# Kernel optimization log

Measured on AMD Instinct MI355X. Metric: run time of the kernel, lower is better.

The kernel has to match this reference:

```python
import jax, jax.numpy as jnp
import numpy as np

B, S, D, E, K = 4, 4096, 2048, 64, 8
STD = 0.02 / np.sqrt(D)
BIAS_UPDATE_SPEED = 0.001


def setup_inputs() -> dict:
    key = jax.random.key(0)
    k1, k2, k3, k4 = jax.random.split(key, 4)
    return {
        "x": jax.random.normal(k1, (B, S, D), dtype=jnp.float32),
        "Wr": (jax.random.normal(k2, (E, D), dtype=jnp.float32) * STD),
        "Wn": (jax.random.normal(k3, (E, D), dtype=jnp.float32) * STD),
        "bias": jnp.zeros((E,), dtype=jnp.float32),
        "noise_u": jax.random.uniform(k4, (B, S, E), dtype=jnp.float32),
    }


def reference(x, Wr, Wn, bias, noise_u):
    # x: [B,S,D]; Wr, Wn: [E,D]; bias: [E]; noise_u: [B,S,E] uniform(0,1)
    logits = jnp.einsum("bsd,ed->bse", x, Wr)          # router logits
    noisy_logits = jnp.einsum("bsd,ed->bse", x, Wn)    # noise scale logits
    noise = noise_u * jax.nn.softplus(noisy_logits)
    z = noise + logits + bias                           # [B,S,E]

    topk_vals, topk_idx = jax.lax.top_k(z, K)           # [B,S,K]
    neg_inf = jnp.full_like(z, -jnp.inf)
    sparse = jnp.put_along_axis(neg_inf, topk_idx, topk_vals, axis=-1,
                                inplace=False)          # -inf except top-k slots
    probs = jax.nn.softmax(sparse, axis=-1)             # [B,S,E]

    # load-balancing bias update (faithful to source, incl. scalar sum quirk)
    sel_mask = jax.nn.one_hot(topk_idx, E, dtype=jnp.float32).sum(axis=(0, 1, 2))  # [E]
    current_expert_load = sel_mask.sum()                # scalar (as in torch .sum(0) on 1-D)
    total_tokens = B * S * K
    avg_load = total_tokens / E
    load_violation = avg_load - current_expert_load
    new_bias = bias + BIAS_UPDATE_SPEED * jnp.sign(load_violation)

    return probs, topk_idx, new_bias
```

## Files before the change

### kernel.cpp

```cpp
#include <hip/hip_runtime.h>
#include <math.h>

#define BB 4
#define SS 4096
#define DD 2048
#define EE 64
#define KK 8
#define TT_TOTAL (BB*SS)
#define E2 128
#define DK 32
#define NC (DD/DK)

typedef double double2_t __attribute__((ext_vector_type(2)));
typedef double double4_t __attribute__((ext_vector_type(4)));

__device__ __forceinline__ double softplus64(double x) {
    return fmax(x, 0.0) + log1p(exp(-fabs(x)));
}

__device__ __forceinline__ int SW(int c) {
    return c ^ (((c >> 4) & 7) << 1);
}

#define ROW 130

template<int KS>
__launch_bounds__(256, 2)
__global__ void gemm8_kernel(const float* __restrict__ x,
                             const float* __restrict__ Wr,
                             const float* __restrict__ Wn,
                             double* __restrict__ zp)
{
    __shared__ __align__(16) double xs[DK][ROW];
    __shared__ __align__(16) double ws[DK][ROW];

    const int tid   = threadIdx.x;
    const int split = blockIdx.x % KS;
    const int bt    = blockIdx.x / KS;
    const int tok0  = bt * 128;
    const int kbase = split * (DD / KS);
    const int NCH   = (DD / KS) / DK;

    const int stok = tid & 127;
    const int skh  = tid >> 7;
    const int scol = SW(stok);
    const float* xsrc = x + (size_t)(tok0 + stok) * DD + kbase + 16 * skh;
    const float* wsrc = ((stok < EE) ? Wr + (size_t)stok * DD
                                     : Wn + (size_t)(stok - EE) * DD)
                        + kbase + 16 * skh;

    const int og2 = tid & 15;
    const int tg2 = tid >> 4;
    int colx[4], colw[4];
    #pragma unroll
    for (int h = 0; h < 4; ++h) colx[h] = SW(2 * tg2 + 32 * h);
    #pragma unroll
    for (int g = 0; g < 4; ++g) colw[g] = SW(2 * og2 + 32 * g);

    double acc[8][8];
    #pragma unroll
    for (int i = 0; i < 8; ++i)
        #pragma unroll
        for (int j = 0; j < 8; ++j) acc[i][j] = 0.0;

    float4 xr[4], wr[4];
    #pragma unroll
    for (int i = 0; i < 4; ++i) {
        xr[i] = *reinterpret_cast<const float4*>(xsrc + 4 * i);
        wr[i] = *reinterpret_cast<const float4*>(wsrc + 4 * i);
    }

    for (int c = 0; c < NCH; ++c) {
        __syncthreads();

        #pragma unroll
        for (int i = 0; i < 4; ++i) {
            const int k = 16 * skh + 4 * i;
            xs[k+0][scol] = (double)xr[i].x;
            xs[k+1][scol] = (double)xr[i].y;
            xs[k+2][scol] = (double)xr[i].z;
            xs[k+3][scol] = (double)xr[i].w;
            ws[k+0][scol] = (double)wr[i].x;
            ws[k+1][scol] = (double)wr[i].y;
            ws[k+2][scol] = (double)wr[i].z;
            ws[k+3][scol] = (double)wr[i].w;
        }
        __syncthreads();

        if (c + 1 < NCH) {
            const int off = (c + 1) * DK;
            #pragma unroll
            for (int i = 0; i < 4; ++i) {
                xr[i] = *reinterpret_cast<const float4*>(xsrc + off + 4 * i);
                wr[i] = *reinterpret_cast<const float4*>(wsrc + off + 4 * i);
            }
        }

        #pragma unroll 4
        for (int k = 0; k < DK; ++k) {
            double2_t xv[4], wv[4];
            #pragma unroll
            for (int h = 0; h < 4; ++h)
                xv[h] = *reinterpret_cast<const double2_t*>(&xs[k][colx[h]]);
            #pragma unroll
            for (int g = 0; g < 4; ++g)
                wv[g] = *reinterpret_cast<const double2_t*>(&ws[k][colw[g]]);
            #pragma unroll
            for (int h = 0; h < 4; ++h)
                #pragma unroll
                for (int e = 0; e < 2; ++e)
                    #pragma unroll
                    for (int g = 0; g < 4; ++g) {
                        acc[2*h+e][2*g+0] = fma(xv[h][e], wv[g][0], acc[2*h+e][2*g+0]);
                        acc[2*h+e][2*g+1] = fma(xv[h][e], wv[g][1], acc[2*h+e][2*g+1]);
                    }
        }
    }

    double* zbase = zp + (size_t)split * TT_TOTAL * E2;
    #pragma unroll
    for (int h = 0; h < 4; ++h)
        #pragma unroll
        for (int e = 0; e < 2; ++e) {
            const int tok = 2 * tg2 + e + 32 * h;
            double* row = zbase + (size_t)(tok0 + tok) * E2;
            #pragma unroll
            for (int g = 0; g < 4; ++g) {
                double2_t v = {acc[2*h+e][2*g+0], acc[2*h+e][2*g+1]};
                *reinterpret_cast<double2_t*>(&row[2 * og2 + 32 * g]) = v;
            }
        }
}

template<int KS>
__launch_bounds__(256, 4)
__global__ void topk2_kernel(const double* __restrict__ zp,
                             const float* __restrict__ bias,
                             const float* __restrict__ noise_u,
                             float* __restrict__ out_probs,
                             float* __restrict__ out_idx)
{
    const int tid  = threadIdx.x;
    const int wid  = tid >> 6;
    const int lane = tid & 63;
    const int tok0 = blockIdx.x * 32;

    for (int tt = 0; tt < 8; ++tt) {
        const int tok = tok0 + wid * 8 + tt;
        const size_t gtok = (size_t)tok;

        double logit = 0.0, noisy = 0.0;
        #pragma unroll
        for (int s = 0; s < KS; ++s) {
            const double* row = zp + (size_t)s * TT_TOTAL * E2 + (size_t)tok * E2;
            logit += row[lane];
            noisy += row[EE + lane];
        }
        const double zv = (double)noise_u[gtok * EE + lane] * softplus64(noisy)
                          + logit + (double)bias[lane];

        double zw = zv;
        bool   sel = false;
        double m0  = 0.0;
        #pragma unroll
        for (int it = 0; it < KK; ++it) {
            double v  = zw;
            int    ix = lane;
            #pragma unroll
            for (int off = 32; off > 0; off >>= 1) {
                const double ov = __shfl_xor(v, off, 64);
                const int    oi = __shfl_xor(ix, off, 64);
                if (ov > v || (ov == v && oi < ix)) { v = ov; ix = oi; }
            }
            if (it == 0) m0 = v;
            if (lane == ix) { sel = true; zw = -INFINITY; }
            if (lane == 0) out_idx[gtok * KK + it] = (float)ix;
        }

        const double ex = sel ? exp(zv - m0) : 0.0;
        double den = ex;
        #pragma unroll
        for (int off = 32; off > 0; off >>= 1) den += __shfl_xor(den, off, 64);

        out_probs[gtok * EE + lane] = (float)(ex / den);
    }
}

#define BT 32
#define XT 34
#define WT 66

__launch_bounds__(256, 4)
__global__ void gemm_kernel(const float* __restrict__ x,
                            const float* __restrict__ Wr,
                            const float* __restrict__ Wn,
                            double* __restrict__ zout)
{
    __shared__ __align__(16) double xs[DK][XT];
    __shared__ __align__(16) double ws[DK][WT];

    const int tid  = threadIdx.x;
    const int bt   = blockIdx.x >> 1;
    const int be   = blockIdx.x & 1;
    const int tok0 = bt * BT;
    const int e0   = be * 64;

    const int kk = tid & 31;
    const int tq = tid >> 5;
    const float* xsrc[4];
    const float* wsrc[8];
    #pragma unroll
    for (int j = 0; j < 4; ++j)
        xsrc[j] = x + (size_t)(tok0 + 4 * tq + j) * DD + kk;
    #pragma unroll
    for (int j = 0; j < 4; ++j) {
        const int e  = e0 + 4 * tq + j;
        const int e2 = e0 + 32 + 4 * tq + j;
        wsrc[j]     = ((e  < EE) ? Wr + (size_t)e * DD
                                 : Wn + (size_t)(e  - EE) * DD) + kk;
        wsrc[4 + j] = ((e2 < EE) ? Wr + (size_t)e2 * DD
                                 : Wn + (size_t)(e2 - EE) * DD) + kk;
    }

    const int og = tid & 15;
    const int tp = tid >> 4;

    double acc[2][4];
    #pragma unroll
    for (int t = 0; t < 2; ++t)
        #pragma unroll
        for (int i = 0; i < 4; ++i) acc[t][i] = 0.0;

    float xr[4], wr[8];
    #pragma unroll
    for (int j = 0; j < 4; ++j) xr[j] = xsrc[j][0];
    #pragma unroll
    for (int j = 0; j < 8; ++j) wr[j] = wsrc[j][0];

    for (int c = 0; c < NC; ++c) {
        __syncthreads();
        {
            double4_t xv = {(double)xr[0], (double)xr[1], (double)xr[2], (double)xr[3]};
            *reinterpret_cast<double4_t*>(&xs[kk][4 * tq]) = xv;
            double4_t w0 = {(double)wr[0], (double)wr[1], (double)wr[2], (double)wr[3]};
            *reinterpret_cast<double4_t*>(&ws[kk][4 * tq]) = w0;
            double4_t w1 = {(double)wr[4], (double)wr[5], (double)wr[6], (double)wr[7]};
            *reinterpret_cast<double4_t*>(&ws[kk][32 + 4 * tq]) = w1;
        }
        __syncthreads();
        if (c + 1 < NC) {
            const int off = (c + 1) * DK;
            #pragma unroll
            for (int j = 0; j < 4; ++j) xr[j] = xsrc[j][off];
            #pragma unroll
            for (int j = 0; j < 8; ++j) wr[j] = wsrc[j][off];
        }
        #pragma unroll 4
        for (int k = 0; k < DK; ++k) {
            const double2_t xv = *reinterpret_cast<const double2_t*>(&xs[k][2 * tp]);
            const double2_t w0 = *reinterpret_cast<const double2_t*>(&ws[k][2 * og]);
            const double2_t w1 = *reinterpret_cast<const double2_t*>(&ws[k][32 + 2 * og]);
            acc[0][0] = fma(xv.x, w0.x, acc[0][0]);
            acc[0][1] = fma(xv.x, w0.y, acc[0][1]);
            acc[0][2] = fma(xv.x, w1.x, acc[0][2]);
            acc[0][3] = fma(xv.x, w1.y, acc[0][3]);
            acc[1][0] = fma(xv.y, w0.x, acc[1][0]);
            acc[1][1] = fma(xv.y, w0.y, acc[1][1]);
            acc[1][2] = fma(xv.y, w1.x, acc[1][2]);
            acc[1][3] = fma(xv.y, w1.y, acc[1][3]);
        }
    }

    #pragma unroll
    for (int t = 0; t < 2; ++t) {
        const size_t base = (size_t)(tok0 + 2 * tp + t) * E2 + e0;
        double2_t lo = {acc[t][0], acc[t][1]};
        double2_t hi = {acc[t][2], acc[t][3]};
        *reinterpret_cast<double2_t*>(&zout[base + 2 * og])      = lo;
        *reinterpret_cast<double2_t*>(&zout[base + 32 + 2 * og]) = hi;
    }
}

#define F_XT 34
#define F_WR 130
#define F_ZR 130
#define F_SMEM ((DK*F_XT + DK*F_WR)*8)

__launch_bounds__(256, 3)
__global__ void router_kernel(const float* __restrict__ x,
                              const float* __restrict__ Wr,
                              const float* __restrict__ Wn,
                              const float* __restrict__ bias,
                              const float* __restrict__ noise_u,
                              float* __restrict__ out_probs,
                              float* __restrict__ out_idx)
{
    __shared__ __align__(16) char smem_raw[F_SMEM];
    double (*xs)[F_XT] = reinterpret_cast<double(*)[F_XT]>(smem_raw);
    double (*wt)[F_WR] = reinterpret_cast<double(*)[F_WR]>(smem_raw + DK*F_XT*8);
    double (*zbuf)[F_ZR] = reinterpret_cast<double(*)[F_ZR]>(smem_raw);

    const int tid  = threadIdx.x;
    const int tok0 = blockIdx.x * 32;
    const int stok = tid >> 3;
    const int sfi  = tid & 7;
    const float* xsrc = x + (size_t)(tok0 + stok) * DD + sfi * 4;
    const float* wsrc[4];
    #pragma unroll
    for (int it = 0; it < 4; ++it) {
        const int r = it * 32 + stok;
        wsrc[it] = ((r < EE) ? (Wr + (size_t)r * DD)
                             : (Wn + (size_t)(r - EE) * DD)) + sfi * 4;
    }
    const int tg = tid >> 5;
    const int eg = tid & 31;

    double acc[4][4];
    #pragma unroll
    for (int t = 0; t < 4; ++t)
        #pragma unroll
        for (int i = 0; i < 4; ++i) acc[t][i] = 0.0;

    float4 xr  = *reinterpret_cast<const float4*>(xsrc);
    float4 wr0 = *reinterpret_cast<const float4*>(wsrc[0]);
    float4 wr1 = *reinterpret_cast<const float4*>(wsrc[1]);
    float4 wr2 = *reinterpret_cast<const float4*>(wsrc[2]);
    float4 wr3 = *reinterpret_cast<const float4*>(wsrc[3]);

    for (int c = 0; c < NC; ++c) {
        __syncthreads();
        {
            const int k0 = sfi * 4;
            xs[k0+0][stok] = (double)xr.x;  xs[k0+1][stok] = (double)xr.y;
            xs[k0+2][stok] = (double)xr.z;  xs[k0+3][stok] = (double)xr.w;
            wt[k0+0][stok      ] = (double)wr0.x; wt[k0+1][stok      ] = (double)wr0.y;
            wt[k0+2][stok      ] = (double)wr0.z; wt[k0+3][stok      ] = (double)wr0.w;
            wt[k0+0][stok + 32 ] = (double)wr1.x; wt[k0+1][stok + 32 ] = (double)wr1.y;
            wt[k0+2][stok + 32 ] = (double)wr1.z; wt[k0+3][stok + 32 ] = (double)wr1.w;
            wt[k0+0][stok + 64 ] = (double)wr2.x; wt[k0+1][stok + 64 ] = (double)wr2.y;
            wt[k0+2][stok + 64 ] = (double)wr2.z; wt[k0+3][stok + 64 ] = (double)wr2.w;
            wt[k0+0][stok + 96 ] = (double)wr3.x; wt[k0+1][stok + 96 ] = (double)wr3.y;
            wt[k0+2][stok + 96 ] = (double)wr3.z; wt[k0+3][stok + 96 ] = (double)wr3.w;
        }
        __syncthreads();
        if (c + 1 < NC) {
            const int off = (c + 1) * DK;
            xr  = *reinterpret_cast<const float4*>(xsrc + off);
            wr0 = *reinterpret_cast<const float4*>(wsrc[0] + off);
            wr1 = *reinterpret_cast<const float4*>(wsrc[1] + off);
            wr2 = *reinterpret_cast<const float4*>(wsrc[2] + off);
            wr3 = *reinterpret_cast<const float4*>(wsrc[3] + off);
        }
        #pragma unroll 4
        for (int k = 0; k < DK; ++k) {
            const double2_t xv0 = *reinterpret_cast<const double2_t*>(&xs[k][tg * 4]);
            const double2_t xv1 = *reinterpret_cast<const double2_t*>(&xs[k][tg * 4 + 2]);
            const double2_t w0  = *reinterpret_cast<const double2_t*>(&wt[k][2 * eg]);
            const double2_t w1  = *reinterpret_cast<const double2_t*>(&wt[k][64 + 2 * eg]);
            const double xvv[4] = {xv0.x, xv0.y, xv1.x, xv1.y};
            #pragma unroll
            for (int t = 0; t < 4; ++t) {
                acc[t][0] = fma(xvv[t], w0.x, acc[t][0]);
                acc[t][1] = fma(xvv[t], w0.y, acc[t][1]);
                acc[t][2] = fma(xvv[t], w1.x, acc[t][2]);
                acc[t][3] = fma(xvv[t], w1.y, acc[t][3]);
            }
        }
    }
    __syncthreads();
    #pragma unroll
    for (int t = 0; t < 4; ++t) {
        double2_t lo = {acc[t][0], acc[t][1]};
        double2_t hi = {acc[t][2], acc[t][3]};
        *reinterpret_cast<double2_t*>(&zbuf[tg * 4 + t][2 * eg])      = lo;
        *reinterpret_cast<double2_t*>(&zbuf[tg * 4 + t][64 + 2 * eg]) = hi;
    }
    __syncthreads();

    const int wid  = tid >> 6;
    const int lane = tid & 63;
    for (int tt = 0; tt < 8; ++tt) {
        const int tok = wid * 8 + tt;
        const size_t gtok = (size_t)tok0 + tok;
        const double logit = zbuf[tok][lane];
        const double noisy = zbuf[tok][EE + lane];
        const double zv = (double)noise_u[gtok * EE + lane] * softplus64(noisy)
                          + logit + (double)bias[lane];
        double zw = zv;
        bool   sel = false;
        double m0  = 0.0;
        #pragma unroll
        for (int it = 0; it < KK; ++it) {
            double v  = zw;
            int    ix = lane;
            #pragma unroll
            for (int off = 32; off > 0; off >>= 1) {
                const double ov = __shfl_xor(v, off, 64);
                const int    oi = __shfl_xor(ix, off, 64);
                if (ov > v || (ov == v && oi < ix)) { v = ov; ix = oi; }
            }
            if (it == 0) m0 = v;
            if (lane == ix) { sel = true; zw = -INFINITY; }
            if (lane == 0) out_idx[gtok * KK + it] = (float)ix;
        }
        const double ex = sel ? exp(zv - m0) : 0.0;
        double den = ex;
        #pragma unroll
        for (int off = 32; off > 0; off >>= 1) den += __shfl_xor(den, off, 64);
        out_probs[gtok * EE + lane] = (float)(ex / den);
    }
}

__global__ void bias_kernel(const float* __restrict__ bias,
                            float* __restrict__ out_bias)
{
    const int e = threadIdx.x;
    if (e < EE) {
        const double load_violation = (double)(TT_TOTAL * KK) / EE
                                      - (double)(TT_TOTAL * KK);
        const double s = (load_violation > 0.0) ? 1.0
                         : ((load_violation < 0.0) ? -1.0 : 0.0);
        out_bias[e] = bias[e] + (float)(0.001 * s);
    }
}

extern "C" void kernel_launch(void* const* d_in, const int* in_sizes, int n_in,
                              void* d_out, int out_size, void* d_ws, size_t ws_size,
                              hipStream_t stream)
{
    const float* x       = (const float*)d_in[0];
    const float* Wr      = (const float*)d_in[1];
    const float* Wn      = (const float*)d_in[2];
    const float* bias    = (const float*)d_in[3];
    const float* noise_u = (const float*)d_in[4];

    float* out       = (float*)d_out;
    float* out_probs = out;
    float* out_idx   = out + (size_t)TT_TOTAL * EE;
    float* out_bias  = out + (size_t)TT_TOTAL * EE + (size_t)TT_TOTAL * KK;

    const size_t z1 = (size_t)TT_TOTAL * E2 * sizeof(double);

    if (ws_size >= 4 * z1) {
        double* zp = (double*)d_ws;
        gemm8_kernel<4><<<128 * 4, 256, 0, stream>>>(x, Wr, Wn, zp);
        topk2_kernel<4><<<TT_TOTAL / 32, 256, 0, stream>>>(zp, bias, noise_u,
                                                           out_probs, out_idx);
    } else if (ws_size >= 2 * z1) {
        double* zp = (double*)d_ws;
        gemm8_kernel<2><<<128 * 2, 256, 0, stream>>>(x, Wr, Wn, zp);
        topk2_kernel<2><<<TT_TOTAL / 32, 256, 0, stream>>>(zp, bias, noise_u,
                                                           out_probs, out_idx);
    } else if (ws_size >= z1) {
        double* z = (double*)d_ws;
        gemm_kernel<<<(TT_TOTAL / BT) * 2, 256, 0, stream>>>(x, Wr, Wn, z);
        topk2_kernel<1><<<TT_TOTAL / 32, 256, 0, stream>>>(z, bias, noise_u,
                                                           out_probs, out_idx);
    } else {
        router_kernel<<<TT_TOTAL / 32, 256, 0, stream>>>(
            x, Wr, Wn, bias, noise_u, out_probs, out_idx);
    }
    bias_kernel<<<1, 64, 0, stream>>>(bias, out_bias);
}
```

Before: 231.3 us.

## Shrink GEMM token tile to 64, stage fp32 in LDS, raise occupancy

The fp64 router GEMM now works on 64-token tiles instead of 128, which doubles the grid. It stores x and W in shared memory as fp32 and converts them to double in the inner loop. The per-thread accumulator tile drops from 8x8 to 4x8 doubles and launch bounds move from 2 to 4 blocks per CU. The aim is to cut LDS footprint and register pressure so more waves can hide latency. The cost is extra float-to-double conversions in the hot loop, fewer FMAs per LDS read, and more global W traffic per output.

```diff
diff --git a/kernel.cpp b/kernel.cpp
--- a/kernel.cpp
+++ b/kernel.cpp
@@ -22,104 +22,118 @@
     return c ^ (((c >> 4) & 7) << 1);
 }
 
-#define ROW 130
+#define XROWF 66
+#define WROWF 130
 
 template<int KS>
-__launch_bounds__(256, 2)
-__global__ void gemm8_kernel(const float* __restrict__ x,
-                             const float* __restrict__ Wr,
-                             const float* __restrict__ Wn,
-                             double* __restrict__ zp)
-{
-    __shared__ __align__(16) double xs[DK][ROW];
-    __shared__ __align__(16) double ws[DK][ROW];
+__launch_bounds__(256, 4)
+__global__ void gemm64_kernel(const float* __restrict__ x,
+                              const float* __restrict__ Wr,
+                              const float* __restrict__ Wn,
+                              double* __restrict__ zp)
+{
+    __shared__ __align__(16) float xs[DK][XROWF];
+    __shared__ __align__(16) float ws[DK][WROWF];
 
     const int tid   = threadIdx.x;
     const int split = blockIdx.x % KS;
     const int bt    = blockIdx.x / KS;
-    const int tok0  = bt * 128;
+    const int tok0  = bt * 64;
     const int kbase = split * (DD / KS);
     const int NCH   = (DD / KS) / DK;
 
-    const int stok = tid & 127;
-    const int skh  = tid >> 7;
-    const int scol = SW(stok);
-    const float* xsrc = x + (size_t)(tok0 + stok) * DD + kbase + 16 * skh;
-    const float* wsrc = ((stok < EE) ? Wr + (size_t)stok * DD
-                                     : Wn + (size_t)(stok - EE) * DD)
-                        + kbase + 16 * skh;
+    const int xrow = tid & 63;
+    const int xkq  = tid >> 6;
+    const int xc   = SW(xrow);
+    const float* xsrc = x + (size_t)(tok0 + xrow) * DD + kbase + 8 * xkq;
+
+    const int wrow = tid & 127;
+    const int wkh  = tid >> 7;
+    const int wc   = SW(wrow);
+    const float* wsrc = ((wrow < EE) ? Wr + (size_t)wrow * DD
+                                     : Wn + (size_t)(wrow - EE) * DD)
+                        + kbase + 16 * wkh;
 
     const int og2 = tid & 15;
     const int tg2 = tid >> 4;
-    int colx[4], colw[4];
-    #pragma unroll
-    for (int h = 0; h < 4; ++h) colx[h] = SW(2 * tg2 + 32 * h);
-    #pragma unroll
-    for (int g = 0; g < 4; ++g) colw[g] = SW(2 * og2 + 32 * g);
-
-    double acc[8][8];
-    #pragma unroll
-    for (int i = 0; i < 8; ++i)
-        #pragma unroll
-        for (int j = 0; j < 8; ++j) acc[i][j] = 0.0;
-
-    float4 xr[4], wr[4];
-    #pragma unroll
-    for (int i = 0; i < 4; ++i) {
-        xr[i] = *reinterpret_cast<const float4*>(xsrc + 4 * i);
-        wr[i] = *reinterpret_cast<const float4*>(wsrc + 4 * i);
-    }
+    const int cx0 = SW(2 * tg2);
+    const int cx1 = SW(2 * tg2 + 32);
+    int cw[4];
+    #pragma unroll
+    for (int g = 0; g < 4; ++g) cw[g] = SW(2 * og2 + 32 * g);
+
+    double acc[4][8];
+    #pragma unroll
+    for (int t = 0; t < 4; ++t)
+        #pragma unroll
+        for (int o = 0; o < 8; ++o) acc[t][o] = 0.0;
+
+    float4 xa[2], wa[4];
+    #pragma unroll
+    for (int i = 0; i < 2; ++i)
+        xa[i] = *reinterpret_cast<const float4*>(xsrc + 4 * i);
+    #pragma unroll
+    for (int i = 0; i < 4; ++i)
+        wa[i] = *reinterpret_cast<const float4*>(wsrc + 4 * i);
 
     for (int c = 0; c < NCH; ++c) {
         __syncthreads();
 
-        #pragma unroll
-        for (int i = 0; i < 4; ++i) {
-            const int k = 16 * skh + 4 * i;
-            xs[k+0][scol] = (double)xr[i].x;
-            xs[k+1][scol] = (double)xr[i].y;
-            xs[k+2][scol] = (double)xr[i].z;
-            xs[k+3][scol] = (double)xr[i].w;
-            ws[k+0][scol] = (double)wr[i].x;
-            ws[k+1][scol] = (double)wr[i].y;
-            ws[k+2][scol] = (double)wr[i].z;
-            ws[k+3][scol] = (double)wr[i].w;
+        {
+            const int kx = 8 * xkq;
+            xs[kx+0][xc] = xa[0].x;  xs[kx+1][xc] = xa[0].y;
+            xs[kx+2][xc] = xa[0].z;  xs[kx+3][xc] = xa[0].w;
+            xs[kx+4][xc] = xa[1].x;  xs[kx+5][xc] = xa[1].y;
+            xs[kx+6][xc] = xa[1].z;  xs[kx+7][xc] = xa[1].w;
+            const int kw = 16 * wkh;
+            #pragma unroll
+            for (int i = 0; i < 4; ++i) {
+                ws[kw + 4*i + 0][wc] = wa[i].x;
+                ws[kw + 4*i + 1][wc] = wa[i].y;
+                ws[kw + 4*i + 2][wc] = wa[i].z;
+                ws[kw + 4*i + 3][wc] = wa[i].w;
+            }
         }
         __syncthreads();
 
         if (c + 1 < NCH) {
             const int off = (c + 1) * DK;
             #pragma unroll
-            for (int i = 0; i < 4; ++i) {
-                xr[i] = *reinterpret_cast<const float4*>(xsrc + off + 4 * i);
-                wr[i] = *reinterpret_cast<const float4*>(wsrc + off + 4 * i);
-            }
+            for (int i = 0; i < 2; ++i)
+                xa[i] = *reinterpret_cast<const float4*>(xsrc + off + 4 * i);
+            #pragma unroll
+            for (int i = 0; i < 4; ++i)
+                wa[i] = *reinterpret_cast<const float4*>(wsrc + off + 4 * i);
         }
 
         #pragma unroll 4
         for (int k = 0; k < DK; ++k) {
-            double2_t xv[4], wv[4];
-            #pragma unroll
-            for (int h = 0; h < 4; ++h)
-                xv[h] = *reinterpret_cast<const double2_t*>(&xs[k][colx[h]]);
+            const float2 xf0 = *reinterpret_cast<const float2*>(&xs[k][cx0]);
+            const float2 xf1 = *reinterpret_cast<const float2*>(&xs[k][cx1]);
+            float2 wf[4];
             #pragma unroll
             for (int g = 0; g < 4; ++g)
-                wv[g] = *reinterpret_cast<const double2_t*>(&ws[k][colw[g]]);
-            #pragma unroll
-            for (int h = 0; h < 4; ++h)
+                wf[g] = *reinterpret_cast<const float2*>(&ws[k][cw[g]]);
+
+            const double xv[4] = {(double)xf0.x, (double)xf0.y,
+                                  (double)xf1.x, (double)xf1.y};
+            double wv[8];
+            #pragma unroll
+            for (int g = 0; g < 4; ++g) {
+                wv[2*g+0] = (double)wf[g].x;
+                wv[2*g+1] = (double)wf[g].y;
+            }
+            #pragma unroll
+            for (int t = 0; t < 4; ++t)
                 #pragma unroll
-                for (int e = 0; e < 2; ++e)
-                    #pragma unroll
-                    for (int g = 0; g < 4; ++g) {
-                        acc[2*h+e][2*g+0] = fma(xv[h][e], wv[g][0], acc[2*h+e][2*g+0]);
-                        acc[2*h+e][2*g+1] = fma(xv[h][e], wv[g][1], acc[2*h+e][2*g+1]);
-                    }
+                for (int o = 0; o < 8; ++o)
+                    acc[t][o] = fma(xv[t], wv[o], acc[t][o]);
         }
     }
 
     double* zbase = zp + (size_t)split * TT_TOTAL * E2;
     #pragma unroll
-    for (int h = 0; h < 4; ++h)
+    for (int h = 0; h < 2; ++h)
         #pragma unroll
         for (int e = 0; e < 2; ++e) {
             const int tok = 2 * tg2 + e + 32 * h;
@@ -443,12 +457,12 @@
 
     if (ws_size >= 4 * z1) {
         double* zp = (double*)d_ws;
-        gemm8_kernel<4><<<128 * 4, 256, 0, stream>>>(x, Wr, Wn, zp);
+        gemm64_kernel<4><<<256 * 4, 256, 0, stream>>>(x, Wr, Wn, zp);
         topk2_kernel<4><<<TT_TOTAL / 32, 256, 0, stream>>>(zp, bias, noise_u,
                                                            out_probs, out_idx);
     } else if (ws_size >= 2 * z1) {
         double* zp = (double*)d_ws;
-        gemm8_kernel<2><<<128 * 2, 256, 0, stream>>>(x, Wr, Wn, zp);
+        gemm64_kernel<2><<<256 * 2, 256, 0, stream>>>(x, Wr, Wn, zp);
         topk2_kernel<2><<<TT_TOTAL / 32, 256, 0, stream>>>(zp, bias, noise_u,
                                                            out_probs, out_idx);
     } else if (ws_size >= z1) {
```

New measurement: 278.1 us. +20.3%, slower.

## Double-buffer shared-memory tiles in fp64 router GEMM with two-stage prefetch

Applied to the files above, without the earlier changes.

The GEMM kernel now keeps two half-size (16-deep) shared-memory tiles. While it computes on one buffer it writes the next chunk into the other and issues global loads two chunks ahead. This removes one of the two barriers per chunk and lets LDS stores overlap with FMA work. In exchange the chunk loop runs twice as many iterations, each with less work per barrier, and register pressure may rise.

```diff
diff --git a/kernel.cpp b/kernel.cpp
--- a/kernel.cpp
+++ b/kernel.cpp
@@ -22,32 +22,33 @@
     return c ^ (((c >> 4) & 7) << 1);
 }
 
+#define DKH 16
 #define ROW 130
 
 template<int KS>
 __launch_bounds__(256, 2)
-__global__ void gemm8_kernel(const float* __restrict__ x,
-                             const float* __restrict__ Wr,
-                             const float* __restrict__ Wn,
-                             double* __restrict__ zp)
-{
-    __shared__ __align__(16) double xs[DK][ROW];
-    __shared__ __align__(16) double ws[DK][ROW];
+__global__ void gemm8d_kernel(const float* __restrict__ x,
+                              const float* __restrict__ Wr,
+                              const float* __restrict__ Wn,
+                              double* __restrict__ zp)
+{
+    __shared__ __align__(16) double xs[2][DKH][ROW];
+    __shared__ __align__(16) double ws[2][DKH][ROW];
 
     const int tid   = threadIdx.x;
     const int split = blockIdx.x % KS;
     const int bt    = blockIdx.x / KS;
     const int tok0  = bt * 128;
     const int kbase = split * (DD / KS);
-    const int NCH   = (DD / KS) / DK;
-
-    const int stok = tid & 127;
+    const int NCH   = (DD / KS) / DKH;
+
+    const int srow = tid & 127;
     const int skh  = tid >> 7;
-    const int scol = SW(stok);
-    const float* xsrc = x + (size_t)(tok0 + stok) * DD + kbase + 16 * skh;
-    const float* wsrc = ((stok < EE) ? Wr + (size_t)stok * DD
-                                     : Wn + (size_t)(stok - EE) * DD)
-                        + kbase + 16 * skh;
+    const int scol = SW(srow);
+    const float* xsrc = x + (size_t)(tok0 + srow) * DD + kbase + 8 * skh;
+    const float* wsrc = ((srow < EE) ? Wr + (size_t)srow * DD
+                                     : Wn + (size_t)(srow - EE) * DD)
+                        + kbase + 8 * skh;
 
     const int og2 = tid & 15;
     const int tg2 = tid >> 4;
@@ -63,48 +64,62 @@
         #pragma unroll
         for (int j = 0; j < 8; ++j) acc[i][j] = 0.0;
 
-    float4 xr[4], wr[4];
-    #pragma unroll
-    for (int i = 0; i < 4; ++i) {
-        xr[i] = *reinterpret_cast<const float4*>(xsrc + 4 * i);
-        wr[i] = *reinterpret_cast<const float4*>(wsrc + 4 * i);
-    }
+    float4 xa0, xa1, wa0, wa1;
+
+    xa0 = *reinterpret_cast<const float4*>(xsrc);
+    xa1 = *reinterpret_cast<const float4*>(xsrc + 4);
+    wa0 = *reinterpret_cast<const float4*>(wsrc);
+    wa1 = *reinterpret_cast<const float4*>(wsrc + 4);
+    {
+        const int k0 = 8 * skh;
+        xs[0][k0+0][scol] = (double)xa0.x;  xs[0][k0+1][scol] = (double)xa0.y;
+        xs[0][k0+2][scol] = (double)xa0.z;  xs[0][k0+3][scol] = (double)xa0.w;
+        xs[0][k0+4][scol] = (double)xa1.x;  xs[0][k0+5][scol] = (double)xa1.y;
+        xs[0][k0+6][scol] = (double)xa1.z;  xs[0][k0+7][scol] = (double)xa1.w;
+        ws[0][k0+0][scol] = (double)wa0.x;  ws[0][k0+1][scol] = (double)wa0.y;
+        ws[0][k0+2][scol] = (double)wa0.z;  ws[0][k0+3][scol] = (double)wa0.w;
+        ws[0][k0+4][scol] = (double)wa1.x;  ws[0][k0+5][scol] = (double)wa1.y;
+        ws[0][k0+6][scol] = (double)wa1.z;  ws[0][k0+7][scol] = (double)wa1.w;
+    }
+    if (NCH > 1) {
+        xa0 = *reinterpret_cast<const float4*>(xsrc + DKH);
+        xa1 = *reinterpret_cast<const float4*>(xsrc + DKH + 4);
+        wa0 = *reinterpret_cast<const float4*>(wsrc + DKH);
+        wa1 = *reinterpret_cast<const float4*>(wsrc + DKH + 4);
+    }
+    __syncthreads();
 
     for (int c = 0; c < NCH; ++c) {
-        __syncthreads();
-
-        #pragma unroll
-        for (int i = 0; i < 4; ++i) {
-            const int k = 16 * skh + 4 * i;
-            xs[k+0][scol] = (double)xr[i].x;
-            xs[k+1][scol] = (double)xr[i].y;
-            xs[k+2][scol] = (double)xr[i].z;
-            xs[k+3][scol] = (double)xr[i].w;
-            ws[k+0][scol] = (double)wr[i].x;
-            ws[k+1][scol] = (double)wr[i].y;
-            ws[k+2][scol] = (double)wr[i].z;
-            ws[k+3][scol] = (double)wr[i].w;
-        }
-        __syncthreads();
+        const int b = c & 1;
 
         if (c + 1 < NCH) {
-            const int off = (c + 1) * DK;
-            #pragma unroll
-            for (int i = 0; i < 4; ++i) {
-                xr[i] = *reinterpret_cast<const float4*>(xsrc + off + 4 * i);
-                wr[i] = *reinterpret_cast<const float4*>(wsrc + off + 4 * i);
-            }
+            const int k0 = 8 * skh;
+            xs[b^1][k0+0][scol] = (double)xa0.x;  xs[b^1][k0+1][scol] = (double)xa0.y;
+            xs[b^1][k0+2][scol] = (double)xa0.z;  xs[b^1][k0+3][scol] = (double)xa0.w;
+            xs[b^1][k0+4][scol] = (double)xa1.x;  xs[b^1][k0+5][scol] = (double)xa1.y;
+            xs[b^1][k0+6][scol] = (double)xa1.z;  xs[b^1][k0+7][scol] = (double)xa1.w;
+            ws[b^1][k0+0][scol] = (double)wa0.x;  ws[b^1][k0+1][scol] = (double)wa0.y;
+            ws[b^1][k0+2][scol] = (double)wa0.z;  ws[b^1][k0+3][scol] = (double)wa0.w;
+            ws[b^1][k0+4][scol] = (double)wa1.x;  ws[b^1][k0+5][scol] = (double)wa1.y;
+            ws[b^1][k0+6][scol] = (double)wa1.z;  ws[b^1][k0+7][scol] = (double)wa1.w;
+        }
+        if (c + 2 < NCH) {
+            const int off = (c + 2) * DKH;
+            xa0 = *reinterpret_cast<const float4*>(xsrc + off);
+            xa1 = *reinterpret_cast<const float4*>(xsrc + off + 4);
+            wa0 = *reinterpret_cast<const float4*>(wsrc + off);
+            wa1 = *reinterpret_cast<const float4*>(wsrc + off + 4);
         }
 
         #pragma unroll 4
-        for (int k = 0; k < DK; ++k) {
+        for (int k = 0; k < DKH; ++k) {
             double2_t xv[4], wv[4];
             #pragma unroll
             for (int h = 0; h < 4; ++h)
-                xv[h] = *reinterpret_cast<const double2_t*>(&xs[k][colx[h]]);
+                xv[h] = *reinterpret_cast<const double2_t*>(&xs[b][k][colx[h]]);
             #pragma unroll
             for (int g = 0; g < 4; ++g)
-                wv[g] = *reinterpret_cast<const double2_t*>(&ws[k][colw[g]]);
+                wv[g] = *reinterpret_cast<const double2_t*>(&ws[b][k][colw[g]]);
             #pragma unroll
             for (int h = 0; h < 4; ++h)
                 #pragma unroll
@@ -115,6 +130,7 @@
                         acc[2*h+e][2*g+1] = fma(xv[h][e], wv[g][1], acc[2*h+e][2*g+1]);
                     }
         }
+        __syncthreads();
     }
 
     double* zbase = zp + (size_t)split * TT_TOTAL * E2;
@@ -443,12 +459,12 @@
 
     if (ws_size >= 4 * z1) {
         double* zp = (double*)d_ws;
-        gemm8_kernel<4><<<128 * 4, 256, 0, stream>>>(x, Wr, Wn, zp);
+        gemm8d_kernel<4><<<128 * 4, 256, 0, stream>>>(x, Wr, Wn, zp);
         topk2_kernel<4><<<TT_TOTAL / 32, 256, 0, stream>>>(zp, bias, noise_u,
                                                            out_probs, out_idx);
     } else if (ws_size >= 2 * z1) {
         double* zp = (double*)d_ws;
-        gemm8_kernel<2><<<128 * 2, 256, 0, stream>>>(x, Wr, Wn, zp);
+        gemm8d_kernel<2><<<128 * 2, 256, 0, stream>>>(x, Wr, Wn, zp);
         topk2_kernel<2><<<TT_TOTAL / 32, 256, 0, stream>>>(zp, bias, noise_u,
                                                            out_probs, out_idx);
     } else if (ws_size >= z1) {
```

Measured after the change: 236.6 us. 2.3% more time.
